# Kernel optimization log

Measured on AMD Instinct MI355X. Metric: run time of the kernel, lower is better.

## Reference

```python
import jax, jax.numpy as jnp
import numpy as np

B, U, L, H = 2048, 512, 32, 64  # batch, num_units, latent_dim, hidden


def setup_inputs() -> dict:
    key = jax.random.key(0)
    ks = jax.random.split(key, 17)
    s = 0.05  # weight scale
    inp = {
        "x": jax.random.normal(ks[0], (B, U), dtype=jnp.float32),
        # encoder: U -> 64 -> 64 -> 64 -> L
        "We1": jax.random.normal(ks[1], (U, H), jnp.float32) * s,
        "be1": jnp.zeros((H,), jnp.float32),
        "We2": jax.random.normal(ks[2], (H, H), jnp.float32) * s,
        "be2": jnp.zeros((H,), jnp.float32),
        "We3": jax.random.normal(ks[3], (H, H), jnp.float32) * s,
        "be3": jnp.zeros((H,), jnp.float32),
        "We4": jax.random.normal(ks[4], (H, L), jnp.float32) * s,
        "be4": jnp.zeros((L,), jnp.float32),
        # U disjoint decoders, weights stacked along unit axis: L -> 64 -> 64 -> 64 -> 1
        "Wd1": jax.random.normal(ks[5], (U, L, H), jnp.float32) * s,
        "bd1": jnp.zeros((U, H), jnp.float32),
        "Wd2": jax.random.normal(ks[6], (U, H, H), jnp.float32) * s,
        "bd2": jnp.zeros((U, H), jnp.float32),
        "Wd3": jax.random.normal(ks[7], (U, H, H), jnp.float32) * s,
        "bd3": jnp.zeros((U, H), jnp.float32),
        "Wd4": jax.random.normal(ks[8], (U, H), jnp.float32) * s,  # last layer out_dim=1, squeezed
        "bd4": jnp.zeros((U,), jnp.float32),
    }
    return inp


def reference(x, We1, be1, We2, be2, We3, be3, We4, be4,
              Wd1, bd1, Wd2, bd2, Wd3, bd3, Wd4, bd4):
    # shared encoder MLP: [B, U] -> [B, L]
    z = jax.nn.relu(x @ We1 + be1)
    z = jax.nn.relu(z @ We2 + be2)
    z = jax.nn.relu(z @ We3 + be3)
    z = z @ We4 + be4  # [B, L]
    # all U decoders batched as grouped GEMMs: [B, L] -> [B, U]
    h = jax.nn.relu(jnp.einsum('bl,ulh->buh', z, Wd1) + bd1)   # [B, U, H]
    h = jax.nn.relu(jnp.einsum('buh,uhk->buk', h, Wd2) + bd2)  # [B, U, H]
    h = jax.nn.relu(jnp.einsum('buh,uhk->buk', h, Wd3) + bd3)  # [B, U, H]
    out = jnp.einsum('buh,uh->bu', h, Wd4) + bd4               # [B, U]
    return out
```

## Files before the change

kernel.cpp:

```cpp
#include <hip/hip_runtime.h>
#include <hip/hip_bf16.h>
#include <hip/hip_fp16.h>
#include <stdint.h>

#define NB 2048
#define NU 512
#define NL 32
#define NH 64

typedef float    f4    __attribute__((ext_vector_type(4)));
typedef uint32_t u32x4 __attribute__((ext_vector_type(4)));
typedef _Float16 h8    __attribute__((ext_vector_type(8)));
typedef _Float16 h2    __attribute__((ext_vector_type(2)));

__device__ __forceinline__ f4 mfma16h(u32x4 a, u32x4 b, f4 c) {
    return __builtin_amdgcn_mfma_f32_16x16x32_f16(
        __builtin_bit_cast(h8, a), __builtin_bit_cast(h8, b), c, 0, 0, 0);
}

__device__ __forceinline__ uint32_t pk2h(float a, float b) {
    uint32_t la = (uint32_t)__half_as_ushort(__float2half_rn(a));
    uint32_t hb = (uint32_t)__half_as_ushort(__float2half_rn(b));
    return la | (hb << 16);
}

__device__ __forceinline__ uint32_t pk_rtz(float e, float o) {
    return __builtin_bit_cast(uint32_t, __builtin_amdgcn_cvt_pkrtz(e, o));
}

__device__ __forceinline__ uint32_t pk_relu(float e, float o) {
    uint32_t r = pk_rtz(e, o);
    asm("v_pk_max_f16 %0, %1, 0" : "=v"(r) : "v"(r));
    return r;
}

__device__ __forceinline__ float dot2(uint32_t a, uint32_t b, float c) {
    return __builtin_amdgcn_fdot2(__builtin_bit_cast(h2, a),
                                  __builtin_bit_cast(h2, b), c, false);
}

__device__ __forceinline__ float red_lg(float x) {
    float a = x, b = x;
    asm("v_permlane16_swap_b32 %0, %1" : "+v"(a), "+v"(b));
    x = a + b;
    a = x; b = x;
    asm("v_permlane32_swap_b32 %0, %1" : "+v"(a), "+v"(b));
    return a + b;
}

__global__ __launch_bounds__(512)
void enc_kernel(const float* __restrict__ x,
                const float* __restrict__ We1, const float* __restrict__ be1,
                const float* __restrict__ We2, const float* __restrict__ be2,
                const float* __restrict__ We3, const float* __restrict__ be3,
                const float* __restrict__ We4, const float* __restrict__ be4,
                uint32_t* __restrict__ zpk)
{
    const int RE = 8;
    __shared__ float xs[RE][512];
    __shared__ float ws[128 * 64];
    __shared__ float h[RE][NH];
    __shared__ float h2s[RE][NH];

    const int t  = threadIdx.x;
    const int r0 = blockIdx.x * RE;

    {
        const f4* xv  = (const f4*)(x + (size_t)r0 * 512);
        f4*       xsv = (f4*)&xs[0][0];
        for (int i = t; i < RE * 512 / 4; i += 512) xsv[i] = xv[i];
    }

    const int j = t & 63;
    const int w = t >> 6;

    float acc0 = be1[j];
    for (int kc = 0; kc < 512; kc += 128) {
        __syncthreads();
        const f4* wv  = (const f4*)(We1 + (size_t)kc * 64);
        f4*       wsv = (f4*)ws;
        for (int i = t; i < 128 * 64 / 4; i += 512) wsv[i] = wv[i];
        __syncthreads();
        #pragma unroll 8
        for (int k = 0; k < 128; ++k)
            acc0 = fmaf(xs[w][kc + k], ws[k * 64 + j], acc0);
    }
    acc0 = fmaxf(acc0, 0.f);
    __syncthreads();
    h[w][j] = acc0;
    __syncthreads();

    acc0 = be2[j];
    #pragma unroll
    for (int k = 0; k < 64; ++k)
        acc0 = fmaf(h[w][k], We2[k * 64 + j], acc0);
    acc0 = fmaxf(acc0, 0.f);
    h2s[w][j] = acc0;
    __syncthreads();

    acc0 = be3[j];
    #pragma unroll
    for (int k = 0; k < 64; ++k)
        acc0 = fmaf(h2s[w][k], We3[k * 64 + j], acc0);
    acc0 = fmaxf(acc0, 0.f);
    h[w][j] = acc0;
    __syncthreads();

    if (t < 256) {
        const int j4  = t & 31;
        const int row = t >> 5;
        float acc = be4[j4];
        #pragma unroll
        for (int k = 0; k < 64; ++k)
            acc = fmaf(h[row][k], We4[k * 32 + j4], acc);
        float nb = __shfl_xor(acc, 1);
        if ((j4 & 1) == 0)
            zpk[(size_t)(r0 + row) * 16 + (j4 >> 1)] = pk2h(acc, nb);
    }
}

template <int K2>
__device__ __forceinline__ void stageW(const float* __restrict__ g,
                                       uint32_t (*dst)[68], int t)
{
    for (int g4 = t; g4 < K2 * 16; g4 += 256) {
        const int k2 = g4 >> 4, c4 = (g4 & 15) << 2;
        f4 a = *(const f4*)(g + (size_t)(2 * k2) * NH + c4);
        f4 b = *(const f4*)(g + (size_t)(2 * k2 + 1) * NH + c4);
        u32x4 p;
        p[0] = pk2h(a[0], b[0]);
        p[1] = pk2h(a[1], b[1]);
        p[2] = pk2h(a[2], b[2]);
        p[3] = pk2h(a[3], b[3]);
        *(u32x4*)&dst[k2][c4] = p;
    }
}

__global__ __launch_bounds__(256)
void dec_kernel(const uint32_t* __restrict__ zpk,
                const float* __restrict__ Wd1, const float* __restrict__ bd1,
                const float* __restrict__ Wd2, const float* __restrict__ bd2,
                const float* __restrict__ Wd3, const float* __restrict__ bd3,
                const float* __restrict__ Wd4, const float* __restrict__ bd4,
                float* __restrict__ out)
{
    __shared__ uint32_t wpk1[16][68];
    __shared__ uint32_t wpk2[32][68];
    __shared__ uint32_t wpk3[150][68];
    __shared__ float bsh[3][NH];
    __shared__ float w4s[NH];

    const int bid = blockIdx.x;
    const int u = ((bid & 7) << 4) | (((bid >> 3) & 3) << 7) | (bid >> 5);
    const int t = threadIdx.x;

    stageW<16>(Wd1 + (size_t)u * NL * NH, wpk1, t);
    stageW<32>(Wd2 + (size_t)u * NH * NH, wpk2, t);
    stageW<32>(Wd3 + (size_t)u * NH * NH, wpk3, t);
    if (t < NH) {
        bsh[0][t] = bd1[(size_t)u * NH + t];
        bsh[1][t] = bd2[(size_t)u * NH + t];
        bsh[2][t] = bd3[(size_t)u * NH + t];
        w4s[t]    = Wd4[(size_t)u * NH + t];
    }
    __syncthreads();

    const int w  = t >> 6;
    const int lr = t & 15;
    const int lg = (t & 63) >> 4;
    const float b4 = bd4[u];

    int cperm[4];
    #pragma unroll
    for (int mt = 0; mt < 4; ++mt)
        cperm[mt] = ((mt >> 1) << 5) + ((lr >> 2) << 3) + ((mt & 1) << 2) + (lr & 3);

    u32x4 a1[4], a2[4][2], a3[4][2];
    #pragma unroll
    for (int mt = 0; mt < 4; ++mt) {
        const int c = cperm[mt];
        #pragma unroll
        for (int i = 0; i < 4; ++i)
            a1[mt][i] = wpk1[lg * 4 + i][c];
        #pragma unroll
        for (int ks = 0; ks < 2; ++ks) {
            #pragma unroll
            for (int i = 0; i < 4; ++i) {
                a2[mt][ks][i] = wpk2[ks * 16 + lg * 4 + i][c];
                a3[mt][ks][i] = wpk3[ks * 16 + lg * 4 + i][c];
            }
        }
    }

    int bq[4];
    #pragma unroll
    for (int mt = 0; mt < 4; ++mt)
        bq[mt] = ((mt >> 1) << 5) + (lg << 3) + ((mt & 1) << 2);

    uint32_t wd4pk[4][2];
    #pragma unroll
    for (int mt = 0; mt < 4; ++mt) {
        wd4pk[mt][0] = pk2h(w4s[bq[mt]],     w4s[bq[mt] + 1]);
        wd4pk[mt][1] = pk2h(w4s[bq[mt] + 2], w4s[bq[mt] + 3]);
    }

    const int rl = w * 16 + lr;

    u32x4 zc[4];
    #pragma unroll
    for (int s = 0; s < 4; ++s)
        zc[s] = *(const u32x4*)(zpk + (size_t)(rl + s * 64) * 16 + lg * 4);

    for (int it = 0; it < 8; ++it) {
        const int rb  = it * 256 + rl;
        const int rbn = ((it + 1) & 7) * 256 + rl;

        f4 acc[4][4];

        {
            f4 c0 = *(const f4*)&bsh[0][bq[0]];
            f4 c1 = *(const f4*)&bsh[0][bq[1]];
            f4 c2 = *(const f4*)&bsh[0][bq[2]];
            f4 c3 = *(const f4*)&bsh[0][bq[3]];
            #pragma unroll
            for (int s = 0; s < 4; ++s) {
                acc[s][0] = mfma16h(a1[0], zc[s], c0);
                acc[s][1] = mfma16h(a1[1], zc[s], c1);
                acc[s][2] = mfma16h(a1[2], zc[s], c2);
                acc[s][3] = mfma16h(a1[3], zc[s], c3);
            }
        }

        u32x4 zn[4];
        #pragma unroll
        for (int s = 0; s < 4; ++s)
            zn[s] = *(const u32x4*)(zpk + (size_t)(rbn + s * 64) * 16 + lg * 4);

        f4 bc2[4], bc3[4];
        #pragma unroll
        for (int mt = 0; mt < 4; ++mt) {
            bc2[mt] = *(const f4*)&bsh[1][bq[mt]];
            bc3[mt] = *(const f4*)&bsh[2][bq[mt]];
        }
        #pragma unroll
        for (int s = 0; s < 4; ++s) {
            u32x4 bf0, bf1;
            bf0[0] = pk_relu(acc[s][0][0], acc[s][0][1]);
            bf0[1] = pk_relu(acc[s][0][2], acc[s][0][3]);
            bf0[2] = pk_relu(acc[s][1][0], acc[s][1][1]);
            bf0[3] = pk_relu(acc[s][1][2], acc[s][1][3]);
            bf1[0] = pk_relu(acc[s][2][0], acc[s][2][1]);
            bf1[1] = pk_relu(acc[s][2][2], acc[s][2][3]);
            bf1[2] = pk_relu(acc[s][3][0], acc[s][3][1]);
            bf1[3] = pk_relu(acc[s][3][2], acc[s][3][3]);

            #pragma unroll
            for (int mt = 0; mt < 4; ++mt)
                acc[s][mt] = mfma16h(a2[mt][0], bf0, bc2[mt]);
            #pragma unroll
            for (int mt = 0; mt < 4; ++mt)
                acc[s][mt] = mfma16h(a2[mt][1], bf1, acc[s][mt]);

            bf0[0] = pk_relu(acc[s][0][0], acc[s][0][1]);
            bf0[1] = pk_relu(acc[s][0][2], acc[s][0][3]);
            bf0[2] = pk_relu(acc[s][1][0], acc[s][1][1]);
            bf0[3] = pk_relu(acc[s][1][2], acc[s][1][3]);
            bf1[0] = pk_relu(acc[s][2][0], acc[s][2][1]);
            bf1[1] = pk_relu(acc[s][2][2], acc[s][2][3]);
            bf1[2] = pk_relu(acc[s][3][0], acc[s][3][1]);
            bf1[3] = pk_relu(acc[s][3][2], acc[s][3][3]);

            #pragma unroll
            for (int mt = 0; mt < 4; ++mt)
                acc[s][mt] = mfma16h(a3[mt][0], bf0, bc3[mt]);
            #pragma unroll
            for (int mt = 0; mt < 4; ++mt)
                acc[s][mt] = mfma16h(a3[mt][1], bf1, acc[s][mt]);
        }

        #pragma unroll
        for (int s = 0; s < 4; ++s) {
            float pa = 0.f, pb = 0.f;
            #pragma unroll
            for (int mt = 0; mt < 4; ++mt) {
                uint32_t p0 = pk_relu(acc[s][mt][0], acc[s][mt][1]);
                uint32_t p1 = pk_relu(acc[s][mt][2], acc[s][mt][3]);
                pa = dot2(p0, wd4pk[mt][0], pa);
                pb = dot2(p1, wd4pk[mt][1], pb);
            }
            float part = red_lg(pa + pb);
            if ((t & 48) == 0)
                out[(size_t)(rb + s * 64) * NU + u] = part + b4;
        }

        #pragma unroll
        for (int s = 0; s < 4; ++s) zc[s] = zn[s];
    }
}

extern "C" void kernel_launch(void* const* d_in, const int* in_sizes, int n_in,
                              void* d_out, int out_size, void* d_ws, size_t ws_size,
                              hipStream_t stream)
{
    const float* x   = (const float*)d_in[0];
    const float* We1 = (const float*)d_in[1];
    const float* be1 = (const float*)d_in[2];
    const float* We2 = (const float*)d_in[3];
    const float* be2 = (const float*)d_in[4];
    const float* We3 = (const float*)d_in[5];
    const float* be3 = (const float*)d_in[6];
    const float* We4 = (const float*)d_in[7];
    const float* be4 = (const float*)d_in[8];
    const float* Wd1 = (const float*)d_in[9];
    const float* bd1 = (const float*)d_in[10];
    const float* Wd2 = (const float*)d_in[11];
    const float* bd2 = (const float*)d_in[12];
    const float* Wd3 = (const float*)d_in[13];
    const float* bd3 = (const float*)d_in[14];
    const float* Wd4 = (const float*)d_in[15];
    const float* bd4 = (const float*)d_in[16];
    float* out = (float*)d_out;

    uint32_t* zpk = (uint32_t*)d_ws;

    enc_kernel<<<NB / 8, 512, 0, stream>>>(x, We1, be1, We2, be2, We3, be3,
                                           We4, be4, zpk);
    dec_kernel<<<NU, 256, 0, stream>>>(zpk, Wd1, bd1, Wd2, bd2,
                                       Wd3, bd3, Wd4, bd4, out);
}
```

Before: 44.59 us.

## Switch decoder MLP to 32x32x16 MFMA tiles with permuted feature layout

Rewrites the per-unit decoder loop to use 32x32x16 f16 MFMA instructions instead of 16x16x32, processing 32 batch rows per wave per iteration. Feature columns and biases are permuted so each layer's accumulator maps directly onto the next layer's B operand, and the final reduction needs only one cross-lane swap. The z prefetch double-buffering is dropped, and layer-1 bias is reloaded from LDS via volatile reads every iteration. Larger MFMA tiles aim to cut instruction count and cross-lane reduction, at the cost of less latency hiding on z loads and a different register footprint.

```diff
diff --git a/kernel.cpp b/kernel.cpp
--- a/kernel.cpp
+++ b/kernel.cpp
@@ -8,13 +8,16 @@
 #define NL 32
 #define NH 64
 
-typedef float    f4    __attribute__((ext_vector_type(4)));
-typedef uint32_t u32x4 __attribute__((ext_vector_type(4)));
-typedef _Float16 h8    __attribute__((ext_vector_type(8)));
-typedef _Float16 h2    __attribute__((ext_vector_type(2)));
-
-__device__ __forceinline__ f4 mfma16h(u32x4 a, u32x4 b, f4 c) {
-    return __builtin_amdgcn_mfma_f32_16x16x32_f16(
+typedef float    f4     __attribute__((ext_vector_type(4)));
+typedef float    f32x16 __attribute__((ext_vector_type(16)));
+typedef uint32_t u32x4  __attribute__((ext_vector_type(4)));
+typedef _Float16 h8     __attribute__((ext_vector_type(8)));
+typedef _Float16 h2     __attribute__((ext_vector_type(2)));
+
+union C16 { f32x16 v; f4 q[4]; };
+
+__device__ __forceinline__ f32x16 mfma32h(u32x4 a, u32x4 b, f32x16 c) {
+    return __builtin_amdgcn_mfma_f32_32x32x16_f16(
         __builtin_bit_cast(h8, a), __builtin_bit_cast(h8, b), c, 0, 0, 0);
 }
 
@@ -37,15 +40,6 @@
 __device__ __forceinline__ float dot2(uint32_t a, uint32_t b, float c) {
     return __builtin_amdgcn_fdot2(__builtin_bit_cast(h2, a),
                                   __builtin_bit_cast(h2, b), c, false);
-}
-
-__device__ __forceinline__ float red_lg(float x) {
-    float a = x, b = x;
-    asm("v_permlane16_swap_b32 %0, %1" : "+v"(a), "+v"(b));
-    x = a + b;
-    a = x; b = x;
-    asm("v_permlane32_swap_b32 %0, %1" : "+v"(a), "+v"(b));
-    return a + b;
 }
 
 __global__ __launch_bounds__(512)
@@ -147,8 +141,9 @@
     __shared__ uint32_t wpk1[16][68];
     __shared__ uint32_t wpk2[32][68];
     __shared__ uint32_t wpk3[150][68];
-    __shared__ float bsh[3][NH];
+    __shared__ float bsh2[NH], bsh3[NH];
     __shared__ float w4s[NH];
+    __shared__ float bshp1[64];
 
     const int bid = blockIdx.x;
     const int u = ((bid & 7) << 4) | (((bid >> 3) & 3) << 7) | (bid >> 5);
@@ -158,144 +153,142 @@
     stageW<32>(Wd2 + (size_t)u * NH * NH, wpk2, t);
     stageW<32>(Wd3 + (size_t)u * NH * NH, wpk3, t);
     if (t < NH) {
-        bsh[0][t] = bd1[(size_t)u * NH + t];
-        bsh[1][t] = bd2[(size_t)u * NH + t];
-        bsh[2][t] = bd3[(size_t)u * NH + t];
-        w4s[t]    = Wd4[(size_t)u * NH + t];
-    }
-    __syncthreads();
-
-    const int w  = t >> 6;
-    const int lr = t & 15;
-    const int lg = (t & 63) >> 4;
+        bsh2[t] = bd2[(size_t)u * NH + t];
+        bsh3[t] = bd3[(size_t)u * NH + t];
+        w4s[t]  = Wd4[(size_t)u * NH + t];
+        const int tt = t >> 5, hh = (t >> 4) & 1, rg = t & 15;
+        const int ft = ((2 * tt + ((rg >> 2) & 1)) << 4) + (hh << 3) +
+                       (((rg >> 3) & 1) << 2) + (rg & 3);
+        bshp1[t] = bd1[(size_t)u * NH + ft];
+    }
+    __syncthreads();
+
+    const int lane = t & 63;
+    const int w    = t >> 6;
+    const int c    = lane & 31;
+    const int h    = lane >> 5;
     const float b4 = bd4[u];
 
-    int cperm[4];
-    #pragma unroll
-    for (int mt = 0; mt < 4; ++mt)
-        cperm[mt] = ((mt >> 1) << 5) + ((lr >> 2) << 3) + ((mt & 1) << 2) + (lr & 3);
-
-    u32x4 a1[4], a2[4][2], a3[4][2];
-    #pragma unroll
-    for (int mt = 0; mt < 4; ++mt) {
-        const int c = cperm[mt];
+    const int fc0 = (((c >> 3) & 1) << 4) + (((c >> 2) & 1) << 3) +
+                    (((c >> 4) & 1) << 2) + (c & 3);
+    const int fc1 = fc0 + 32;
+
+    u32x4 a1[2][2], a2[2][4], a3[2][4];
+    #pragma unroll
+    for (int ks = 0; ks < 2; ++ks)
         #pragma unroll
-        for (int i = 0; i < 4; ++i)
-            a1[mt][i] = wpk1[lg * 4 + i][c];
+        for (int i = 0; i < 4; ++i) {
+            a1[0][ks][i] = wpk1[8 * ks + 4 * h + i][fc0];
+            a1[1][ks][i] = wpk1[8 * ks + 4 * h + i][fc1];
+        }
+    #pragma unroll
+    for (int ks = 0; ks < 4; ++ks)
         #pragma unroll
-        for (int ks = 0; ks < 2; ++ks) {
-            #pragma unroll
-            for (int i = 0; i < 4; ++i) {
-                a2[mt][ks][i] = wpk2[ks * 16 + lg * 4 + i][c];
-                a3[mt][ks][i] = wpk3[ks * 16 + lg * 4 + i][c];
-            }
-        }
-    }
-
-    int bq[4];
-    #pragma unroll
-    for (int mt = 0; mt < 4; ++mt)
-        bq[mt] = ((mt >> 1) << 5) + (lg << 3) + ((mt & 1) << 2);
-
-    uint32_t wd4pk[4][2];
-    #pragma unroll
-    for (int mt = 0; mt < 4; ++mt) {
-        wd4pk[mt][0] = pk2h(w4s[bq[mt]],     w4s[bq[mt] + 1]);
-        wd4pk[mt][1] = pk2h(w4s[bq[mt] + 2], w4s[bq[mt] + 3]);
-    }
-
-    const int rl = w * 16 + lr;
-
-    u32x4 zc[4];
-    #pragma unroll
-    for (int s = 0; s < 4; ++s)
-        zc[s] = *(const u32x4*)(zpk + (size_t)(rl + s * 64) * 16 + lg * 4);
-
-    for (int it = 0; it < 8; ++it) {
-        const int rb  = it * 256 + rl;
-        const int rbn = ((it + 1) & 7) * 256 + rl;
-
-        f4 acc[4][4];
-
+        for (int i = 0; i < 4; ++i) {
+            a2[0][ks][i] = wpk2[8 * ks + 4 * h + i][fc0];
+            a2[1][ks][i] = wpk2[8 * ks + 4 * h + i][fc1];
+            a3[0][ks][i] = wpk3[8 * ks + 4 * h + i][fc0];
+            a3[1][ks][i] = wpk3[8 * ks + 4 * h + i][fc1];
+        }
+
+    f32x16 c2a, c2b, c3a, c3b;
+    #pragma unroll
+    for (int rg = 0; rg < 16; ++rg) {
+        const int fA = (((rg >> 2) & 1) << 4) + (h << 3) +
+                       (((rg >> 3) & 1) << 2) + (rg & 3);
+        c2a[rg] = bsh2[fA];  c2b[rg] = bsh2[fA + 32];
+        c3a[rg] = bsh3[fA];  c3b[rg] = bsh3[fA + 32];
+    }
+
+    uint32_t wd4pk[4][4];
+    #pragma unroll
+    for (int j = 0; j < 4; ++j)
+        #pragma unroll
+        for (int ww = 0; ww < 4; ++ww) {
+            const int f0 = 16 * j + 8 * h + 2 * ww;
+            wd4pk[j][ww] = pk2h(w4s[f0], w4s[f0 + 1]);
+        }
+
+    #define PACKBF(A_, B_)                                                   \
+        bf0[0] = pk_relu(A_[0], A_[1]);   bf0[1] = pk_relu(A_[2], A_[3]);    \
+        bf0[2] = pk_relu(A_[8], A_[9]);   bf0[3] = pk_relu(A_[10], A_[11]);  \
+        bf1[0] = pk_relu(A_[4], A_[5]);   bf1[1] = pk_relu(A_[6], A_[7]);    \
+        bf1[2] = pk_relu(A_[12], A_[13]); bf1[3] = pk_relu(A_[14], A_[15]);  \
+        bf2[0] = pk_relu(B_[0], B_[1]);   bf2[1] = pk_relu(B_[2], B_[3]);    \
+        bf2[2] = pk_relu(B_[8], B_[9]);   bf2[3] = pk_relu(B_[10], B_[11]);  \
+        bf3[0] = pk_relu(B_[4], B_[5]);   bf3[1] = pk_relu(B_[6], B_[7]);    \
+        bf3[2] = pk_relu(B_[12], B_[13]); bf3[3] = pk_relu(B_[14], B_[15]);
+
+    for (int it = 0; it < 16; ++it) {
+        const int row = it * 128 + w * 32 + c;
+        const u32x4 zlo = *(const u32x4*)(zpk + (size_t)row * 16 + 4 * h);
+        const u32x4 zhi = *(const u32x4*)(zpk + (size_t)row * 16 + 8 + 4 * h);
+
+        C16 c1a, c1b;
         {
-            f4 c0 = *(const f4*)&bsh[0][bq[0]];
-            f4 c1 = *(const f4*)&bsh[0][bq[1]];
-            f4 c2 = *(const f4*)&bsh[0][bq[2]];
-            f4 c3 = *(const f4*)&bsh[0][bq[3]];
-            #pragma unroll
-            for (int s = 0; s < 4; ++s) {
-                acc[s][0] = mfma16h(a1[0], zc[s], c0);
-                acc[s][1] = mfma16h(a1[1], zc[s], c1);
-                acc[s][2] = mfma16h(a1[2], zc[s], c2);
-                acc[s][3] = mfma16h(a1[3], zc[s], c3);
-            }
-        }
-
-        u32x4 zn[4];
-        #pragma unroll
-        for (int s = 0; s < 4; ++s)
-            zn[s] = *(const u32x4*)(zpk + (size_t)(rbn + s * 64) * 16 + lg * 4);
-
-        f4 bc2[4], bc3[4];
-        #pragma unroll
-        for (int mt = 0; mt < 4; ++mt) {
-            bc2[mt] = *(const f4*)&bsh[1][bq[mt]];
-            bc3[mt] = *(const f4*)&bsh[2][bq[mt]];
-        }
-        #pragma unroll
-        for (int s = 0; s < 4; ++s) {
-            u32x4 bf0, bf1;
-            bf0[0] = pk_relu(acc[s][0][0], acc[s][0][1]);
-            bf0[1] = pk_relu(acc[s][0][2], acc[s][0][3]);
-            bf0[2] = pk_relu(acc[s][1][0], acc[s][1][1]);
-            bf0[3] = pk_relu(acc[s][1][2], acc[s][1][3]);
-            bf1[0] = pk_relu(acc[s][2][0], acc[s][2][1]);
-            bf1[1] = pk_relu(acc[s][2][2], acc[s][2][3]);
-            bf1[2] = pk_relu(acc[s][3][0], acc[s][3][1]);
-            bf1[3] = pk_relu(acc[s][3][2], acc[s][3][3]);
-
-            #pragma unroll
-            for (int mt = 0; mt < 4; ++mt)
-                acc[s][mt] = mfma16h(a2[mt][0], bf0, bc2[mt]);
-            #pragma unroll
-            for (int mt = 0; mt < 4; ++mt)
-                acc[s][mt] = mfma16h(a2[mt][1], bf1, acc[s][mt]);
-
-            bf0[0] = pk_relu(acc[s][0][0], acc[s][0][1]);
-            bf0[1] = pk_relu(acc[s][0][2], acc[s][0][3]);
-            bf0[2] = pk_relu(acc[s][1][0], acc[s][1][1]);
-            bf0[3] = pk_relu(acc[s][1][2], acc[s][1][3]);
-            bf1[0] = pk_relu(acc[s][2][0], acc[s][2][1]);
-            bf1[1] = pk_relu(acc[s][2][2], acc[s][2][3]);
-            bf1[2] = pk_relu(acc[s][3][0], acc[s][3][1]);
-            bf1[3] = pk_relu(acc[s][3][2], acc[s][3][3]);
-
-            #pragma unroll
-            for (int mt = 0; mt < 4; ++mt)
-                acc[s][mt] = mfma16h(a3[mt][0], bf0, bc3[mt]);
-            #pragma unroll
-            for (int mt = 0; mt < 4; ++mt)
-                acc[s][mt] = mfma16h(a3[mt][1], bf1, acc[s][mt]);
-        }
-
-        #pragma unroll
-        for (int s = 0; s < 4; ++s) {
-            float pa = 0.f, pb = 0.f;
-            #pragma unroll
-            for (int mt = 0; mt < 4; ++mt) {
-                uint32_t p0 = pk_relu(acc[s][mt][0], acc[s][mt][1]);
-                uint32_t p1 = pk_relu(acc[s][mt][2], acc[s][mt][3]);
-                pa = dot2(p0, wd4pk[mt][0], pa);
-                pb = dot2(p1, wd4pk[mt][1], pb);
-            }
-            float part = red_lg(pa + pb);
-            if ((t & 48) == 0)
-                out[(size_t)(rb + s * 64) * NU + u] = part + b4;
-        }
-
-        #pragma unroll
-        for (int s = 0; s < 4; ++s) zc[s] = zn[s];
-    }
+            volatile const f4* bv = (volatile const f4*)bshp1;
+            c1a.q[0] = bv[4 * h + 0]; c1a.q[1] = bv[4 * h + 1];
+            c1a.q[2] = bv[4 * h + 2]; c1a.q[3] = bv[4 * h + 3];
+            c1b.q[0] = bv[8 + 4 * h + 0]; c1b.q[1] = bv[8 + 4 * h + 1];
+            c1b.q[2] = bv[8 + 4 * h + 2]; c1b.q[3] = bv[8 + 4 * h + 3];
+        }
+
+        f32x16 accA = mfma32h(a1[0][0], zlo, c1a.v);
+        f32x16 accB = mfma32h(a1[1][0], zlo, c1b.v);
+        accA = mfma32h(a1[0][1], zhi, accA);
+        accB = mfma32h(a1[1][1], zhi, accB);
+
+        u32x4 bf0, bf1, bf2, bf3;
+        PACKBF(accA, accB)
+
+        accA = mfma32h(a2[0][0], bf0, c2a);
+        accB = mfma32h(a2[1][0], bf0, c2b);
+        accA = mfma32h(a2[0][1], bf1, accA);
+        accB = mfma32h(a2[1][1], bf1, accB);
+        accA = mfma32h(a2[0][2], bf2, accA);
+        accB = mfma32h(a2[1][2], bf2, accB);
+        accA = mfma32h(a2[0][3], bf3, accA);
+        accB = mfma32h(a2[1][3], bf3, accB);
+
+        PACKBF(accA, accB)
+
+        accA = mfma32h(a3[0][0], bf0, c3a);
+        accB = mfma32h(a3[1][0], bf0, c3b);
+        accA = mfma32h(a3[0][1], bf1, accA);
+        accB = mfma32h(a3[1][1], bf1, accB);
+        accA = mfma32h(a3[0][2], bf2, accA);
+        accB = mfma32h(a3[1][2], bf2, accB);
+        accA = mfma32h(a3[0][3], bf3, accA);
+        accB = mfma32h(a3[1][3], bf3, accB);
+
+        float pa = 0.f, pb = 0.f, pc = 0.f, pd = 0.f;
+        pa = dot2(pk_relu(accA[0], accA[1]),   wd4pk[0][0], pa);
+        pa = dot2(pk_relu(accA[2], accA[3]),   wd4pk[0][1], pa);
+        pa = dot2(pk_relu(accA[8], accA[9]),   wd4pk[0][2], pa);
+        pa = dot2(pk_relu(accA[10], accA[11]), wd4pk[0][3], pa);
+        pb = dot2(pk_relu(accA[4], accA[5]),   wd4pk[1][0], pb);
+        pb = dot2(pk_relu(accA[6], accA[7]),   wd4pk[1][1], pb);
+        pb = dot2(pk_relu(accA[12], accA[13]), wd4pk[1][2], pb);
+        pb = dot2(pk_relu(accA[14], accA[15]), wd4pk[1][3], pb);
+        pc = dot2(pk_relu(accB[0], accB[1]),   wd4pk[2][0], pc);
+        pc = dot2(pk_relu(accB[2], accB[3]),   wd4pk[2][1], pc);
+        pc = dot2(pk_relu(accB[8], accB[9]),   wd4pk[2][2], pc);
+        pc = dot2(pk_relu(accB[10], accB[11]), wd4pk[2][3], pc);
+        pd = dot2(pk_relu(accB[4], accB[5]),   wd4pk[3][0], pd);
+        pd = dot2(pk_relu(accB[6], accB[7]),   wd4pk[3][1], pd);
+        pd = dot2(pk_relu(accB[12], accB[13]), wd4pk[3][2], pd);
+        pd = dot2(pk_relu(accB[14], accB[15]), wd4pk[3][3], pd);
+
+        float part = (pa + pb) + (pc + pd);
+        {
+            float aa = part, bb = part;
+            asm("v_permlane32_swap_b32 %0, %1" : "+v"(aa), "+v"(bb));
+            part = aa + bb;
+        }
+        if (h == 0)
+            out[(size_t)row * NU + u] = part + b4;
+    }
+    #undef PACKBF
 }
 
 extern "C" void kernel_launch(void* const* d_in, const int* in_sizes, int n_in,
```

After: 57.67 us. 1.29x slower.
